# Kernel optimization log

Measured on AMD Instinct MI355X. Metric: run time of the kernel, lower is better.

## Reference

```python
import jax, jax.numpy as jnp
import numpy as np

K = 5
EPS = 1e-08


def setup_inputs() -> dict:
    key = jax.random.key(0)
    x = jax.random.normal(key, (8192, 512), dtype=jnp.float32)
    return {"x": x}


def reference(x):
    n = x.shape[0]
    # torch: everything below through topk is under no_grad, and x is rebound
    # to the normalized tensor, so the whole graph is detached from the input.
    xn = x / jnp.linalg.norm(x, axis=1, keepdims=True)
    xn = jax.lax.stop_gradient(xn)
    dots = xn @ xn.T                                  # [N, N]
    dots = jnp.where(jnp.eye(n, dtype=bool), jnp.float32(-1.0), dots)
    _, topk_idx = jax.lax.top_k(dots, K)              # [N, K]
    x_neighbors = xn[topk_idx]                        # [N, K, D]
    diffs = xn[:, None, :] - x_neighbors              # [N, K, D]
    distances = jnp.linalg.norm(diffs, axis=-1)       # [N, K]
    mean_rho = distances.mean(axis=1)                 # [N]
    loss = -jnp.mean(jnp.log(mean_rho + EPS))
    return loss
```

## Files before the change

### kernel.cpp

```cpp
#include <hip/hip_runtime.h>
#include <math.h>

#define NROWS 8192
#define DIM   512
#define KNN   5
#define EPSV  1e-8f

#define BM 128
#define BN 128
#define BK 32
#define NT (NROWS / BM)
#define NT64 (NROWS / 64)
#define NKS (DIM / BK)
#define NWORK 2080

typedef __attribute__((ext_vector_type(8))) _Float16 f16x8;
typedef __attribute__((ext_vector_type(4))) float    f32x4;

__device__ __forceinline__ void gload16(const _Float16* g, _Float16* l) {
    __builtin_amdgcn_global_load_lds(
        (const __attribute__((address_space(1))) void*)g,
        (__attribute__((address_space(3))) void*)l, 16, 0, 0);
}

__device__ __forceinline__ void cmpswap(float& a, float& b) {
    const float hi = fmaxf(a, b), lo = fminf(a, b);
    a = hi; b = lo;
}

__device__ __forceinline__ void merge5(float a[KNN], const float b[KNN]) {
    const float c0 = fmaxf(a[0], b[0]);
    const float c1 = fmaxf(fmaxf(a[1], b[1]), fminf(a[0], b[0]));
    const float c2 = fmaxf(fmaxf(a[2], b[2]),
                           fmaxf(fminf(a[0], b[1]), fminf(a[1], b[0])));
    const float c3 = fmaxf(fmaxf(a[3], b[3]),
                           fmaxf(fminf(a[0], b[2]),
                                 fmaxf(fminf(a[1], b[1]), fminf(a[2], b[0]))));
    const float c4 = fmaxf(fmaxf(a[4], b[4]),
                           fmaxf(fmaxf(fminf(a[0], b[3]), fminf(a[1], b[2])),
                                 fmaxf(fminf(a[2], b[1]), fminf(a[3], b[0]))));
    a[0] = c0; a[1] = c1; a[2] = c2; a[3] = c3; a[4] = c4;
}

__global__ __launch_bounds__(256) void norm_kernel(const float* __restrict__ x,
                                                   _Float16* __restrict__ xnh,
                                                   float* __restrict__ out) {
    const int wv = threadIdx.x >> 6, lane = threadIdx.x & 63;
    const int row = blockIdx.x * 4 + wv;
    const float4* xr = (const float4*)(x + (size_t)row * DIM) + lane * 2;
    const float4 a = xr[0];
    const float4 b = xr[1];
    float s = a.x * a.x + a.y * a.y + a.z * a.z + a.w * a.w
            + b.x * b.x + b.y * b.y + b.z * b.z + b.w * b.w;
    #pragma unroll
    for (int off = 1; off < 64; off <<= 1) s += __shfl_xor(s, off, 64);
    const float inv = 1.0f / sqrtf(s);
    const f16x8 h = { (_Float16)(a.x * inv), (_Float16)(a.y * inv),
                      (_Float16)(a.z * inv), (_Float16)(a.w * inv),
                      (_Float16)(b.x * inv), (_Float16)(b.y * inv),
                      (_Float16)(b.z * inv), (_Float16)(b.w * inv) };
    *(f16x8*)(xnh + (size_t)row * DIM + lane * 8) = h;

    if (blockIdx.x == 0 && threadIdx.x == 0) *out = 0.f;
}

__global__ __launch_bounds__(256) void dots_top3_kernel(const _Float16* __restrict__ xnh,
                                                        float* __restrict__ M3) {
    int I, J;
    {
        int rem = (int)(blockIdx.x & 7) * (NWORK / 8) + (int)(blockIdx.x >> 3);
        int found = 0;
        for (int SI = 0; SI < 8 && !found; ++SI) {
            for (int SJ = SI; SJ < 8 && !found; ++SJ) {
                const int sz = (SI == SJ) ? 36 : 64;
                if (rem < sz) {
                    if (SI == SJ) {
                        int i = 0, r2 = rem;
                        while (r2 >= 8 - i) { r2 -= 8 - i; ++i; }
                        I = SI * 8 + i;
                        J = SJ * 8 + i + r2;
                    } else {
                        I = SI * 8 + (rem >> 3);
                        J = SJ * 8 + (rem & 7);
                    }
                    found = 1;
                } else {
                    rem -= sz;
                }
            }
        }
    }

    __shared__ __align__(16) _Float16 As[BM * BK];
    __shared__ __align__(16) _Float16 Bs[BN * BK];

    const int tid    = threadIdx.x;
    const int lane   = tid & 63;
    const int wv     = tid >> 6;
    const int wm     = wv >> 1;
    const int wn     = wv & 1;
    const int m_lane = lane & 15;
    const int quad   = lane >> 4;

    const int i0 = I * BM;
    const int j0 = J * BN;

    const int rowlocal = (m_lane >> 2) * 16 + quad * 4 + (m_lane & 3);
    const int myrow    = i0 + wm * 64 + rowlocal;

    const int rchunk = (quad ^ ((m_lane >> 1) & 3)) * 8;

    f32x4 acc[4][4];
    #pragma unroll
    for (int m = 0; m < 4; ++m)
        #pragma unroll
        for (int n = 0; n < 4; ++n)
            acc[m][n] = (f32x4){0.f, 0.f, 0.f, 0.f};

    for (int ks = 0; ks < NKS; ++ks) {
        const int k0 = ks * BK;
        #pragma unroll
        for (int q = 0; q < 2; ++q) {
            const int s  = tid + q * 256;
            const int r  = s >> 2;
            const int kg = (s & 3) ^ ((s >> 3) & 3);
            gload16(xnh + (size_t)(i0 + r) * DIM + k0 + kg * 8, As + s * 8);
            gload16(xnh + (size_t)(j0 + r) * DIM + k0 + kg * 8, Bs + s * 8);
        }
        __syncthreads();

        f16x8 af[4], bf[4];
        #pragma unroll
        for (int m = 0; m < 4; ++m)
            af[m] = *(const f16x8*)(As + (wm * 64 + m * 16 + m_lane) * BK + rchunk);
        #pragma unroll
        for (int n = 0; n < 4; ++n)
            bf[n] = *(const f16x8*)(Bs + (wn * 64 + n * 16 + m_lane) * BK + rchunk);
        #pragma unroll
        for (int m = 0; m < 4; ++m)
            #pragma unroll
            for (int n = 0; n < 4; ++n)
                acc[m][n] = __builtin_amdgcn_mfma_f32_16x16x32_f16(af[m], bf[n], acc[m][n], 0, 0, 0);
        __syncthreads();
    }

    const bool diag = (I == J) && (wm == wn);
    #pragma unroll
    for (int m = 0; m < 4; ++m)
        #pragma unroll
        for (int i = 0; i < 4; ++i)
            acc[m][m][i] = (diag && (quad * 4 + i) == m_lane) ? -2.f : acc[m][m][i];

    float g1 = -2.f, g2 = -2.f, g3 = -2.f;
    #pragma unroll
    for (int m = 0; m < 4; ++m) {
        #pragma unroll
        for (int i = 0; i < 4; ++i) {
            float v0 = acc[m][0][i], v1 = acc[m][1][i];
            float v2 = acc[m][2][i], v3 = acc[m][3][i];
            cmpswap(v0, v1); cmpswap(v2, v3);
            cmpswap(v0, v2); cmpswap(v1, v3);
            cmpswap(v1, v2);
            float a1 = v0, a2 = v1, a3 = v2;
            #pragma unroll
            for (int d = 1; d < 16; d <<= 1) {
                const float b1 = __shfl_xor(a1, d, 64);
                const float b2 = __shfl_xor(a2, d, 64);
                const float b3 = __shfl_xor(a3, d, 64);
                const float n1 = fmaxf(a1, b1);
                const float n2 = fmaxf(fminf(a1, b1), fmaxf(a2, b2));
                const float n3 = fmaxf(fmaxf(a3, b3),
                                       fmaxf(fminf(a1, b2), fminf(a2, b1)));
                a1 = n1; a2 = n2; a3 = n3;
            }
            const bool own = (m_lane == m * 4 + i);
            g1 = own ? a1 : g1; g2 = own ? a2 : g2; g3 = own ? a3 : g3;
        }
    }
    {
        float* p = M3 + ((size_t)myrow * NT64 + (J * 2 + wn)) * 3;
        p[0] = g1; p[1] = g2; p[2] = g3;
    }

    if (I != J) {
        #pragma unroll
        for (int n = 0; n < 4; ++n) {
            float c1 = -2.f, c2 = -2.f, c3 = -2.f;
            #pragma unroll
            for (int m = 0; m < 4; ++m)
                #pragma unroll
                for (int i = 0; i < 4; ++i) {
                    const float v  = acc[m][n][i];
                    const float u1 = fminf(c1, v);
                    c1 = fmaxf(c1, v);
                    const float u2 = fminf(c2, u1);
                    c2 = fmaxf(c2, u1);
                    c3 = fmaxf(c3, u2);
                }
            #pragma unroll
            for (int d = 16; d < 64; d <<= 1) {
                const float b1 = __shfl_xor(c1, d, 64);
                const float b2 = __shfl_xor(c2, d, 64);
                const float b3 = __shfl_xor(c3, d, 64);
                const float n2 = fmaxf(fminf(c1, b1), fmaxf(c2, b2));
                const float n3 = fmaxf(fmaxf(c3, b3),
                                       fmaxf(fminf(c1, b2), fminf(c2, b1)));
                c1 = fmaxf(c1, b1); c2 = n2; c3 = n3;
            }
            if (quad == 0) {
                const int col = j0 + wn * 64 + n * 16 + m_lane;
                float* p = M3 + ((size_t)col * NT64 + (I * 2 + wm)) * 3;
                p[0] = c1; p[1] = c2; p[2] = c3;
            }
        }
    }
}

__global__ __launch_bounds__(256) void select_loss_kernel(const _Float16* __restrict__ xnh,
                                                          const float* __restrict__ M3,
                                                          float* __restrict__ out) {
    const int wv = threadIdx.x >> 6, lane = threadIdx.x & 63;
    const int row = blockIdx.x * 4 + wv;
    const float* p = M3 + (size_t)row * NT64 * 3 + lane * 6;
    float a[3], b[3];
    a[0] = p[0]; a[1] = p[1]; a[2] = p[2];
    b[0] = p[3]; b[1] = p[4]; b[2] = p[5];

    float t[KNN];
    {
        float c[KNN] = { a[0], a[1], a[2], -2.f, -2.f };
        const float bb[KNN] = { b[0], b[1], b[2], -2.f, -2.f };
        merge5(c, bb);
        #pragma unroll
        for (int d = 1; d < 64; d <<= 1) {
            float o[KNN];
            #pragma unroll
            for (int k = 0; k < KNN; ++k) o[k] = __shfl_xor(c[k], d, 64);
            merge5(c, o);
        }
        #pragma unroll
        for (int k = 0; k < KNN; ++k) t[k] = c[k];
    }

    const unsigned long long ba = __ballot(a[2] >= t[4]);
    const unsigned long long bb_ = __ballot(b[2] >= t[4]);
    if (ba | bb_) {
        const bool fA = (ba >> lane) & 1ull, fB = (bb_ >> lane) & 1ull;
        float c[KNN] = { fA ? -2.f : a[0], fA ? -2.f : a[1], fA ? -2.f : a[2],
                         -2.f, -2.f };
        const float b5[KNN] = { fB ? -2.f : b[0], fB ? -2.f : b[1],
                                fB ? -2.f : b[2], -2.f, -2.f };
        merge5(c, b5);
        #pragma unroll
        for (int d = 1; d < 64; d <<= 1) {
            float o[KNN];
            #pragma unroll
            for (int k = 0; k < KNN; ++k) o[k] = __shfl_xor(c[k], d, 64);
            merge5(c, o);
        }
        #pragma unroll
        for (int k = 0; k < KNN; ++k) t[k] = c[k];

        unsigned long long fl[2] = { ba, bb_ };
        #pragma unroll
        for (int h = 0; h < 2; ++h) {
            unsigned long long m = fl[h];
            while (m) {
                const int l = __ffsll((long long)m) - 1;
                m &= m - 1;
                const int jt2 = 2 * l + h;
                const int col = jt2 * 64 + lane;
                const _Float16* rp = xnh + (size_t)row * DIM;
                const _Float16* cp = xnh + (size_t)col * DIM;
                float d = 0.f;
                for (int k8 = 0; k8 < DIM / 8; ++k8) {
                    const f16x8 rv = *(const f16x8*)(rp + k8 * 8);
                    const f16x8 cv = *(const f16x8*)(cp + k8 * 8);
                    #pragma unroll
                    for (int e = 0; e < 8; ++e)
                        d += (float)rv[e] * (float)cv[e];
                }
                if (col == row) d = -2.f;
                float c2[KNN] = { d, -2.f, -2.f, -2.f, -2.f };
                #pragma unroll
                for (int dd = 1; dd < 64; dd <<= 1) {
                    float o[KNN];
                    #pragma unroll
                    for (int k = 0; k < KNN; ++k) o[k] = __shfl_xor(c2[k], dd, 64);
                    merge5(c2, o);
                }
                merge5(t, c2);
            }
        }
    }

    float s = 0.f;
    #pragma unroll
    for (int k = 0; k < KNN; ++k) s += sqrtf(fmaxf(2.f - 2.f * t[k], 0.f));
    const float val = logf(s * (1.f / KNN) + EPSV);

    __shared__ float red[4];
    if (lane == 0) red[wv] = val;
    __syncthreads();
    if (threadIdx.x == 0) {
        const float blocksum = red[0] + red[1] + red[2] + red[3];
        atomicAdd(out, -blocksum / (float)NROWS);
    }
}

extern "C" void kernel_launch(void* const* d_in, const int* in_sizes, int n_in,
                              void* d_out, int out_size, void* d_ws, size_t ws_size,
                              hipStream_t stream) {
    const float* x = (const float*)d_in[0];
    float* out = (float*)d_out;
    char* ws = (char*)d_ws;

    _Float16* xnh = (_Float16*)ws;
    float* M3 = (float*)(ws + (size_t)NROWS * DIM * sizeof(_Float16));

    norm_kernel<<<NROWS / 4, 256, 0, stream>>>(x, xnh, out);
    dots_top3_kernel<<<NWORK, 256, 0, stream>>>(xnh, M3);
    select_loss_kernel<<<NROWS / 4, 256, 0, stream>>>(xnh, M3, out);
}
```

Before: 169.2 us.

## Fuse norm, dots-top3 and selection into one persistent kernel with grid barriers

Merges the three kernels into a single persistent kernel of 256 blocks that uses software grid barriers between the normalization, tiled GEMM top-3 and selection phases. Each block loops over several GEMM tiles and rows, and the final loss comes from a deterministic partial-sum reduction instead of atomics. The aim is to remove launch overhead and inter-kernel gaps. The cost is that only 256 blocks of 256 threads now carry the GEMM phase, which may cut occupancy and latency hiding, and correctness relies on all blocks being co-resident. A memset on the stream resets the barrier counters each call.

```diff
diff --git a/kernel.cpp b/kernel.cpp
--- a/kernel.cpp
+++ b/kernel.cpp
@@ -9,10 +9,10 @@
 #define BM 128
 #define BN 128
 #define BK 32
-#define NT (NROWS / BM)
 #define NT64 (NROWS / 64)
 #define NKS (DIM / BK)
 #define NWORK 2080
+#define NBLK 256
 
 typedef __attribute__((ext_vector_type(8))) _Float16 f16x8;
 typedef __attribute__((ext_vector_type(4))) float    f32x4;
@@ -42,269 +42,319 @@
     a[0] = c0; a[1] = c1; a[2] = c2; a[3] = c3; a[4] = c4;
 }
 
-__global__ __launch_bounds__(256) void norm_kernel(const float* __restrict__ x,
-                                                   _Float16* __restrict__ xnh,
-                                                   float* __restrict__ out) {
-    const int wv = threadIdx.x >> 6, lane = threadIdx.x & 63;
-    const int row = blockIdx.x * 4 + wv;
-    const float4* xr = (const float4*)(x + (size_t)row * DIM) + lane * 2;
-    const float4 a = xr[0];
-    const float4 b = xr[1];
-    float s = a.x * a.x + a.y * a.y + a.z * a.z + a.w * a.w
-            + b.x * b.x + b.y * b.y + b.z * b.z + b.w * b.w;
-    #pragma unroll
-    for (int off = 1; off < 64; off <<= 1) s += __shfl_xor(s, off, 64);
-    const float inv = 1.0f / sqrtf(s);
-    const f16x8 h = { (_Float16)(a.x * inv), (_Float16)(a.y * inv),
-                      (_Float16)(a.z * inv), (_Float16)(a.w * inv),
-                      (_Float16)(b.x * inv), (_Float16)(b.y * inv),
-                      (_Float16)(b.z * inv), (_Float16)(b.w * inv) };
-    *(f16x8*)(xnh + (size_t)row * DIM + lane * 8) = h;
-
-    if (blockIdx.x == 0 && threadIdx.x == 0) *out = 0.f;
-}
-
-__global__ __launch_bounds__(256) void dots_top3_kernel(const _Float16* __restrict__ xnh,
-                                                        float* __restrict__ M3) {
-    int I, J;
-    {
-        int rem = (int)(blockIdx.x & 7) * (NWORK / 8) + (int)(blockIdx.x >> 3);
-        int found = 0;
-        for (int SI = 0; SI < 8 && !found; ++SI) {
-            for (int SJ = SI; SJ < 8 && !found; ++SJ) {
-                const int sz = (SI == SJ) ? 36 : 64;
-                if (rem < sz) {
-                    if (SI == SJ) {
-                        int i = 0, r2 = rem;
-                        while (r2 >= 8 - i) { r2 -= 8 - i; ++i; }
-                        I = SI * 8 + i;
-                        J = SJ * 8 + i + r2;
-                    } else {
-                        I = SI * 8 + (rem >> 3);
-                        J = SJ * 8 + (rem & 7);
-                    }
-                    found = 1;
-                } else {
-                    rem -= sz;
-                }
+__device__ __forceinline__ void grid_barrier(int* cnt, int* gen) {
+    __syncthreads();
+    if (threadIdx.x == 0) {
+        const int g = __hip_atomic_load(gen, __ATOMIC_RELAXED,
+                                        __HIP_MEMORY_SCOPE_AGENT);
+        const int prev = __hip_atomic_fetch_add(cnt, 1, __ATOMIC_ACQ_REL,
+                                                __HIP_MEMORY_SCOPE_AGENT);
+        if (prev == NBLK - 1) {
+            __hip_atomic_store(cnt, 0, __ATOMIC_RELAXED,
+                               __HIP_MEMORY_SCOPE_AGENT);
+            __hip_atomic_store(gen, g + 1, __ATOMIC_RELEASE,
+                               __HIP_MEMORY_SCOPE_AGENT);
+        } else {
+            while (__hip_atomic_load(gen, __ATOMIC_ACQUIRE,
+                                     __HIP_MEMORY_SCOPE_AGENT) == g) {
+                __builtin_amdgcn_s_sleep(8);
             }
         }
     }
+    __syncthreads();
+}
+
+__global__ __launch_bounds__(256) void fused_kernel(const float* __restrict__ x,
+                                                    _Float16* __restrict__ xnh,
+                                                    float* __restrict__ M3,
+                                                    float* __restrict__ partials,
+                                                    int* __restrict__ syncv,
+                                                    float* __restrict__ out) {
+    const int tid  = threadIdx.x;
+    const int lane = tid & 63;
+    const int wv   = tid >> 6;
+    const int bid  = blockIdx.x;
 
     __shared__ __align__(16) _Float16 As[BM * BK];
     __shared__ __align__(16) _Float16 Bs[BN * BK];
-
-    const int tid    = threadIdx.x;
-    const int lane   = tid & 63;
-    const int wv     = tid >> 6;
-    const int wm     = wv >> 1;
-    const int wn     = wv & 1;
-    const int m_lane = lane & 15;
-    const int quad   = lane >> 4;
-
-    const int i0 = I * BM;
-    const int j0 = J * BN;
-
-    const int rowlocal = (m_lane >> 2) * 16 + quad * 4 + (m_lane & 3);
-    const int myrow    = i0 + wm * 64 + rowlocal;
-
-    const int rchunk = (quad ^ ((m_lane >> 1) & 3)) * 8;
-
-    f32x4 acc[4][4];
+    __shared__ float red[4];
+
+    int* cnt = syncv;
+    int* gen = syncv + 1;
+
     #pragma unroll
-    for (int m = 0; m < 4; ++m)
+    for (int t = 0; t < 8; ++t) {
+        const int row = (bid * 4 + wv) + 1024 * t;
+        const float4* xr = (const float4*)(x + (size_t)row * DIM) + lane * 2;
+        const float4 a = xr[0];
+        const float4 b = xr[1];
+        float s = a.x * a.x + a.y * a.y + a.z * a.z + a.w * a.w
+                + b.x * b.x + b.y * b.y + b.z * b.z + b.w * b.w;
         #pragma unroll
-        for (int n = 0; n < 4; ++n)
-            acc[m][n] = (f32x4){0.f, 0.f, 0.f, 0.f};
-
-    for (int ks = 0; ks < NKS; ++ks) {
-        const int k0 = ks * BK;
-        #pragma unroll
-        for (int q = 0; q < 2; ++q) {
-            const int s  = tid + q * 256;
-            const int r  = s >> 2;
-            const int kg = (s & 3) ^ ((s >> 3) & 3);
-            gload16(xnh + (size_t)(i0 + r) * DIM + k0 + kg * 8, As + s * 8);
-            gload16(xnh + (size_t)(j0 + r) * DIM + k0 + kg * 8, Bs + s * 8);
-        }
-        __syncthreads();
-
-        f16x8 af[4], bf[4];
-        #pragma unroll
-        for (int m = 0; m < 4; ++m)
-            af[m] = *(const f16x8*)(As + (wm * 64 + m * 16 + m_lane) * BK + rchunk);
-        #pragma unroll
-        for (int n = 0; n < 4; ++n)
-            bf[n] = *(const f16x8*)(Bs + (wn * 64 + n * 16 + m_lane) * BK + rchunk);
-        #pragma unroll
-        for (int m = 0; m < 4; ++m)
-            #pragma unroll
-            for (int n = 0; n < 4; ++n)
-                acc[m][n] = __builtin_amdgcn_mfma_f32_16x16x32_f16(af[m], bf[n], acc[m][n], 0, 0, 0);
-        __syncthreads();
-    }
-
-    const bool diag = (I == J) && (wm == wn);
-    #pragma unroll
-    for (int m = 0; m < 4; ++m)
-        #pragma unroll
-        for (int i = 0; i < 4; ++i)
-            acc[m][m][i] = (diag && (quad * 4 + i) == m_lane) ? -2.f : acc[m][m][i];
-
-    float g1 = -2.f, g2 = -2.f, g3 = -2.f;
-    #pragma unroll
-    for (int m = 0; m < 4; ++m) {
-        #pragma unroll
-        for (int i = 0; i < 4; ++i) {
-            float v0 = acc[m][0][i], v1 = acc[m][1][i];
-            float v2 = acc[m][2][i], v3 = acc[m][3][i];
-            cmpswap(v0, v1); cmpswap(v2, v3);
-            cmpswap(v0, v2); cmpswap(v1, v3);
-            cmpswap(v1, v2);
-            float a1 = v0, a2 = v1, a3 = v2;
-            #pragma unroll
-            for (int d = 1; d < 16; d <<= 1) {
-                const float b1 = __shfl_xor(a1, d, 64);
-                const float b2 = __shfl_xor(a2, d, 64);
-                const float b3 = __shfl_xor(a3, d, 64);
-                const float n1 = fmaxf(a1, b1);
-                const float n2 = fmaxf(fminf(a1, b1), fmaxf(a2, b2));
-                const float n3 = fmaxf(fmaxf(a3, b3),
-                                       fmaxf(fminf(a1, b2), fminf(a2, b1)));
-                a1 = n1; a2 = n2; a3 = n3;
-            }
-            const bool own = (m_lane == m * 4 + i);
-            g1 = own ? a1 : g1; g2 = own ? a2 : g2; g3 = own ? a3 : g3;
-        }
-    }
+        for (int off = 1; off < 64; off <<= 1) s += __shfl_xor(s, off, 64);
+        const float inv = 1.0f / sqrtf(s);
+        const f16x8 h = { (_Float16)(a.x * inv), (_Float16)(a.y * inv),
+                          (_Float16)(a.z * inv), (_Float16)(a.w * inv),
+                          (_Float16)(b.x * inv), (_Float16)(b.y * inv),
+                          (_Float16)(b.z * inv), (_Float16)(b.w * inv) };
+        *(f16x8*)(xnh + (size_t)row * DIM + lane * 8) = h;
+    }
+
+    grid_barrier(cnt, gen);
+
     {
-        float* p = M3 + ((size_t)myrow * NT64 + (J * 2 + wn)) * 3;
-        p[0] = g1; p[1] = g2; p[2] = g3;
-    }
-
-    if (I != J) {
-        #pragma unroll
-        for (int n = 0; n < 4; ++n) {
-            float c1 = -2.f, c2 = -2.f, c3 = -2.f;
+        const int xcd = bid & 7;
+        const int q   = bid >> 3;
+        const int wm     = wv >> 1;
+        const int wn     = wv & 1;
+        const int m_lane = lane & 15;
+        const int quad   = lane >> 4;
+        const int rowlocal = (m_lane >> 2) * 16 + quad * 4 + (m_lane & 3);
+        const int rchunk   = (quad ^ ((m_lane >> 1) & 3)) * 8;
+        const int s0 = tid, s1 = tid + 256;
+        const int r0g = s0 >> 2, r1g = s1 >> 2;
+        const int kg0 = (s0 & 3) ^ ((s0 >> 3) & 3);
+        const int kg1 = (s1 & 3) ^ ((s1 >> 3) & 3);
+
+        for (int w = xcd * 260 + q; w < xcd * 260 + 260; w += 32) {
+            int I, J;
+            {
+                int rem = w, found = 0;
+                for (int SI = 0; SI < 8 && !found; ++SI) {
+                    for (int SJ = SI; SJ < 8 && !found; ++SJ) {
+                        const int sz = (SI == SJ) ? 36 : 64;
+                        if (rem < sz) {
+                            if (SI == SJ) {
+                                int i = 0, r2 = rem;
+                                while (r2 >= 8 - i) { r2 -= 8 - i; ++i; }
+                                I = SI * 8 + i;
+                                J = SJ * 8 + i + r2;
+                            } else {
+                                I = SI * 8 + (rem >> 3);
+                                J = SJ * 8 + (rem & 7);
+                            }
+                            found = 1;
+                        } else {
+                            rem -= sz;
+                        }
+                    }
+                }
+            }
+
+            const int i0 = I * BM;
+            const int j0 = J * BN;
+            const int myrow = i0 + wm * 64 + rowlocal;
+            const _Float16* gA0 = xnh + (size_t)(i0 + r0g) * DIM + kg0 * 8;
+            const _Float16* gA1 = xnh + (size_t)(i0 + r1g) * DIM + kg1 * 8;
+            const _Float16* gB0 = xnh + (size_t)(j0 + r0g) * DIM + kg0 * 8;
+            const _Float16* gB1 = xnh + (size_t)(j0 + r1g) * DIM + kg1 * 8;
+
+            f32x4 acc[4][4];
             #pragma unroll
             for (int m = 0; m < 4; ++m)
                 #pragma unroll
+                for (int n = 0; n < 4; ++n)
+                    acc[m][n] = (f32x4){0.f, 0.f, 0.f, 0.f};
+
+            for (int ks = 0; ks < NKS; ++ks) {
+                const int k0 = ks * BK;
+                gload16(gA0 + k0, As + s0 * 8);
+                gload16(gA1 + k0, As + s1 * 8);
+                gload16(gB0 + k0, Bs + s0 * 8);
+                gload16(gB1 + k0, Bs + s1 * 8);
+                __syncthreads();
+
+                f16x8 af[4], bf[4];
+                #pragma unroll
+                for (int m = 0; m < 4; ++m)
+                    af[m] = *(const f16x8*)(As + (wm * 64 + m * 16 + m_lane) * BK + rchunk);
+                #pragma unroll
+                for (int n = 0; n < 4; ++n)
+                    bf[n] = *(const f16x8*)(Bs + (wn * 64 + n * 16 + m_lane) * BK + rchunk);
+                #pragma unroll
+                for (int m = 0; m < 4; ++m)
+                    #pragma unroll
+                    for (int n = 0; n < 4; ++n)
+                        acc[m][n] = __builtin_amdgcn_mfma_f32_16x16x32_f16(af[m], bf[n], acc[m][n], 0, 0, 0);
+                __syncthreads();
+            }
+
+            const bool diag = (I == J) && (wm == wn);
+            #pragma unroll
+            for (int m = 0; m < 4; ++m)
+                #pragma unroll
+                for (int i = 0; i < 4; ++i)
+                    acc[m][m][i] = (diag && (quad * 4 + i) == m_lane) ? -2.f : acc[m][m][i];
+
+            float g1 = -2.f, g2 = -2.f, g3 = -2.f;
+            #pragma unroll
+            for (int m = 0; m < 4; ++m) {
+                #pragma unroll
                 for (int i = 0; i < 4; ++i) {
-                    const float v  = acc[m][n][i];
-                    const float u1 = fminf(c1, v);
-                    c1 = fmaxf(c1, v);
-                    const float u2 = fminf(c2, u1);
-                    c2 = fmaxf(c2, u1);
-                    c3 = fmaxf(c3, u2);
-                }
+                    float v0 = acc[m][0][i], v1 = acc[m][1][i];
+                    float v2 = acc[m][2][i], v3 = acc[m][3][i];
+                    cmpswap(v0, v1); cmpswap(v2, v3);
+                    cmpswap(v0, v2); cmpswap(v1, v3);
+                    cmpswap(v1, v2);
+                    float a1 = v0, a2 = v1, a3 = v2;
+                    #pragma unroll
+                    for (int d = 1; d < 16; d <<= 1) {
+                        const float b1 = __shfl_xor(a1, d, 64);
+                        const float b2 = __shfl_xor(a2, d, 64);
+                        const float b3 = __shfl_xor(a3, d, 64);
+                        const float n1 = fmaxf(a1, b1);
+                        const float n2 = fmaxf(fminf(a1, b1), fmaxf(a2, b2));
+                        const float n3 = fmaxf(fmaxf(a3, b3),
+                                               fmaxf(fminf(a1, b2), fminf(a2, b1)));
+                        a1 = n1; a2 = n2; a3 = n3;
+                    }
+                    const bool own = (m_lane == m * 4 + i);
+                    g1 = own ? a1 : g1; g2 = own ? a2 : g2; g3 = own ? a3 : g3;
+                }
+            }
+            {
+                float* p = M3 + ((size_t)myrow * NT64 + (J * 2 + wn)) * 3;
+                p[0] = g1; p[1] = g2; p[2] = g3;
+            }
+
+            if (I != J) {
+                #pragma unroll
+                for (int n = 0; n < 4; ++n) {
+                    float c1 = -2.f, c2 = -2.f, c3 = -2.f;
+                    #pragma unroll
+                    for (int m = 0; m < 4; ++m)
+                        #pragma unroll
+                        for (int i = 0; i < 4; ++i) {
+                            const float v  = acc[m][n][i];
+                            const float u1 = fminf(c1, v);
+                            c1 = fmaxf(c1, v);
+                            const float u2 = fminf(c2, u1);
+                            c2 = fmaxf(c2, u1);
+                            c3 = fmaxf(c3, u2);
+                        }
+                    #pragma unroll
+                    for (int d = 16; d < 64; d <<= 1) {
+                        const float b1 = __shfl_xor(c1, d, 64);
+                        const float b2 = __shfl_xor(c2, d, 64);
+                        const float b3 = __shfl_xor(c3, d, 64);
+                        const float n2 = fmaxf(fminf(c1, b1), fmaxf(c2, b2));
+                        const float n3 = fmaxf(fmaxf(c3, b3),
+                                               fmaxf(fminf(c1, b2), fminf(c2, b1)));
+                        c1 = fmaxf(c1, b1); c2 = n2; c3 = n3;
+                    }
+                    if (quad == 0) {
+                        const int col = j0 + wn * 64 + n * 16 + m_lane;
+                        float* p = M3 + ((size_t)col * NT64 + (I * 2 + wm)) * 3;
+                        p[0] = c1; p[1] = c2; p[2] = c3;
+                    }
+                }
+            }
+        }
+    }
+
+    grid_barrier(cnt, gen);
+
+    {
+        float wsum = 0.f;
+        #pragma unroll
+        for (int t = 0; t < 8; ++t) {
+            const int row = (bid * 4 + wv) + 1024 * t;
+            const float* p = M3 + (size_t)row * NT64 * 3 + lane * 6;
+            float a[3], b[3];
+            a[0] = p[0]; a[1] = p[1]; a[2] = p[2];
+            b[0] = p[3]; b[1] = p[4]; b[2] = p[5];
+
+            float tk[KNN];
+            {
+                float c[KNN] = { a[0], a[1], a[2], -2.f, -2.f };
+                const float bb[KNN] = { b[0], b[1], b[2], -2.f, -2.f };
+                merge5(c, bb);
+                #pragma unroll
+                for (int d = 1; d < 64; d <<= 1) {
+                    float o[KNN];
+                    #pragma unroll
+                    for (int k = 0; k < KNN; ++k) o[k] = __shfl_xor(c[k], d, 64);
+                    merge5(c, o);
+                }
+                #pragma unroll
+                for (int k = 0; k < KNN; ++k) tk[k] = c[k];
+            }
+
+            const unsigned long long ba  = __ballot(a[2] >= tk[4]);
+            const unsigned long long bb_ = __ballot(b[2] >= tk[4]);
+            if (ba | bb_) {
+                const bool fA = (ba >> lane) & 1ull, fB = (bb_ >> lane) & 1ull;
+                float c[KNN] = { fA ? -2.f : a[0], fA ? -2.f : a[1],
+                                 fA ? -2.f : a[2], -2.f, -2.f };
+                const float b5[KNN] = { fB ? -2.f : b[0], fB ? -2.f : b[1],
+                                        fB ? -2.f : b[2], -2.f, -2.f };
+                merge5(c, b5);
+                #pragma unroll
+                for (int d = 1; d < 64; d <<= 1) {
+                    float o[KNN];
+                    #pragma unroll
+                    for (int k = 0; k < KNN; ++k) o[k] = __shfl_xor(c[k], d, 64);
+                    merge5(c, o);
+                }
+                #pragma unroll
+                for (int k = 0; k < KNN; ++k) tk[k] = c[k];
+
+                unsigned long long fl[2] = { ba, bb_ };
+                #pragma unroll
+                for (int h = 0; h < 2; ++h) {
+                    unsigned long long m = fl[h];
+                    while (m) {
+                        const int l = __ffsll((long long)m) - 1;
+                        m &= m - 1;
+                        const int jt2 = 2 * l + h;
+                        const int col = jt2 * 64 + lane;
+                        const _Float16* rp = xnh + (size_t)row * DIM;
+                        const _Float16* cp = xnh + (size_t)col * DIM;
+                        float d = 0.f;
+                        for (int k8 = 0; k8 < DIM / 8; ++k8) {
+                            const f16x8 rv = *(const f16x8*)(rp + k8 * 8);
+                            const f16x8 cv = *(const f16x8*)(cp + k8 * 8);
+                            #pragma unroll
+                            for (int e = 0; e < 8; ++e)
+                                d += (float)rv[e] * (float)cv[e];
+                        }
+                        if (col == row) d = -2.f;
+                        float c2[KNN] = { d, -2.f, -2.f, -2.f, -2.f };
+                        #pragma unroll
+                        for (int dd = 1; dd < 64; dd <<= 1) {
+                            float o[KNN];
+                            #pragma unroll
+                            for (int k = 0; k < KNN; ++k) o[k] = __shfl_xor(c2[k], dd, 64);
+                            merge5(c2, o);
+                        }
+                        merge5(tk, c2);
+                    }
+                }
+            }
+
+            float s = 0.f;
             #pragma unroll
-            for (int d = 16; d < 64; d <<= 1) {
-                const float b1 = __shfl_xor(c1, d, 64);
-                const float b2 = __shfl_xor(c2, d, 64);
-                const float b3 = __shfl_xor(c3, d, 64);
-                const float n2 = fmaxf(fminf(c1, b1), fmaxf(c2, b2));
-                const float n3 = fmaxf(fmaxf(c3, b3),
-                                       fmaxf(fminf(c1, b2), fminf(c2, b1)));
-                c1 = fmaxf(c1, b1); c2 = n2; c3 = n3;
-            }
-            if (quad == 0) {
-                const int col = j0 + wn * 64 + n * 16 + m_lane;
-                float* p = M3 + ((size_t)col * NT64 + (I * 2 + wm)) * 3;
-                p[0] = c1; p[1] = c2; p[2] = c3;
-            }
+            for (int k = 0; k < KNN; ++k) s += sqrtf(fmaxf(2.f - 2.f * tk[k], 0.f));
+            wsum += logf(s * (1.f / KNN) + EPSV);
         }
-    }
-}
-
-__global__ __launch_bounds__(256) void select_loss_kernel(const _Float16* __restrict__ xnh,
-                                                          const float* __restrict__ M3,
-                                                          float* __restrict__ out) {
-    const int wv = threadIdx.x >> 6, lane = threadIdx.x & 63;
-    const int row = blockIdx.x * 4 + wv;
-    const float* p = M3 + (size_t)row * NT64 * 3 + lane * 6;
-    float a[3], b[3];
-    a[0] = p[0]; a[1] = p[1]; a[2] = p[2];
-    b[0] = p[3]; b[1] = p[4]; b[2] = p[5];
-
-    float t[KNN];
-    {
-        float c[KNN] = { a[0], a[1], a[2], -2.f, -2.f };
-        const float bb[KNN] = { b[0], b[1], b[2], -2.f, -2.f };
-        merge5(c, bb);
+
+        if (lane == 0) red[wv] = wsum;
+        __syncthreads();
+        if (tid == 0)
+            partials[bid] = red[0] + red[1] + red[2] + red[3];
+    }
+
+    grid_barrier(cnt, gen);
+
+    if (bid == 0) {
+        float s = partials[tid];
         #pragma unroll
-        for (int d = 1; d < 64; d <<= 1) {
-            float o[KNN];
-            #pragma unroll
-            for (int k = 0; k < KNN; ++k) o[k] = __shfl_xor(c[k], d, 64);
-            merge5(c, o);
-        }
-        #pragma unroll
-        for (int k = 0; k < KNN; ++k) t[k] = c[k];
-    }
-
-    const unsigned long long ba = __ballot(a[2] >= t[4]);
-    const unsigned long long bb_ = __ballot(b[2] >= t[4]);
-    if (ba | bb_) {
-        const bool fA = (ba >> lane) & 1ull, fB = (bb_ >> lane) & 1ull;
-        float c[KNN] = { fA ? -2.f : a[0], fA ? -2.f : a[1], fA ? -2.f : a[2],
-                         -2.f, -2.f };
-        const float b5[KNN] = { fB ? -2.f : b[0], fB ? -2.f : b[1],
-                                fB ? -2.f : b[2], -2.f, -2.f };
-        merge5(c, b5);
-        #pragma unroll
-        for (int d = 1; d < 64; d <<= 1) {
-            float o[KNN];
-            #pragma unroll
-            for (int k = 0; k < KNN; ++k) o[k] = __shfl_xor(c[k], d, 64);
-            merge5(c, o);
-        }
-        #pragma unroll
-        for (int k = 0; k < KNN; ++k) t[k] = c[k];
-
-        unsigned long long fl[2] = { ba, bb_ };
-        #pragma unroll
-        for (int h = 0; h < 2; ++h) {
-            unsigned long long m = fl[h];
-            while (m) {
-                const int l = __ffsll((long long)m) - 1;
-                m &= m - 1;
-                const int jt2 = 2 * l + h;
-                const int col = jt2 * 64 + lane;
-                const _Float16* rp = xnh + (size_t)row * DIM;
-                const _Float16* cp = xnh + (size_t)col * DIM;
-                float d = 0.f;
-                for (int k8 = 0; k8 < DIM / 8; ++k8) {
-                    const f16x8 rv = *(const f16x8*)(rp + k8 * 8);
-                    const f16x8 cv = *(const f16x8*)(cp + k8 * 8);
-                    #pragma unroll
-                    for (int e = 0; e < 8; ++e)
-                        d += (float)rv[e] * (float)cv[e];
-                }
-                if (col == row) d = -2.f;
-                float c2[KNN] = { d, -2.f, -2.f, -2.f, -2.f };
-                #pragma unroll
-                for (int dd = 1; dd < 64; dd <<= 1) {
-                    float o[KNN];
-                    #pragma unroll
-                    for (int k = 0; k < KNN; ++k) o[k] = __shfl_xor(c2[k], dd, 64);
-                    merge5(c2, o);
-                }
-                merge5(t, c2);
-            }
-        }
-    }
-
-    float s = 0.f;
-    #pragma unroll
-    for (int k = 0; k < KNN; ++k) s += sqrtf(fmaxf(2.f - 2.f * t[k], 0.f));
-    const float val = logf(s * (1.f / KNN) + EPSV);
-
-    __shared__ float red[4];
-    if (lane == 0) red[wv] = val;
-    __syncthreads();
-    if (threadIdx.x == 0) {
-        const float blocksum = red[0] + red[1] + red[2] + red[3];
-        atomicAdd(out, -blocksum / (float)NROWS);
+        for (int off = 1; off < 64; off <<= 1) s += __shfl_xor(s, off, 64);
+        __syncthreads();
+        if (lane == 0) red[wv] = s;
+        __syncthreads();
+        if (tid == 0)
+            *out = -(red[0] + red[1] + red[2] + red[3]) / (float)NROWS;
     }
 }
 
@@ -317,8 +367,9 @@
 
     _Float16* xnh = (_Float16*)ws;
     float* M3 = (float*)(ws + (size_t)NROWS * DIM * sizeof(_Float16));
-
-    norm_kernel<<<NROWS / 4, 256, 0, stream>>>(x, xnh, out);
-    dots_top3_kernel<<<NWORK, 256, 0, stream>>>(xnh, M3);
-    select_loss_kernel<<<NROWS / 4, 256, 0, stream>>>(xnh, M3, out);
-}
+    float* partials = M3 + (size_t)NROWS * NT64 * 3;
+    int* syncv = (int*)(partials + NBLK);
+
+    hipMemsetAsync(syncv, 0, 2 * sizeof(int), stream);
+    fused_kernel<<<NBLK, 256, 0, stream>>>(x, xnh, M3, partials, syncv, out);
+}
```

New measurement: 316.1 us. +86.8%, slower.
